# Optimization experiments

Hardware: AMD Instinct MI355X
Metric: run time of the kernel (lower is better)

Reference implementation:

```python
import jax, jax.numpy as jnp
import numpy as np

B, L, Q = 1024, 200, 1
DQ, DF = 512, 128
H, D1, D2 = 4, 128, 64


def setup_inputs() -> dict:
    key = jax.random.key(0)
    ks = jax.random.split(key, 20)
    inp = {
        "query": jax.random.normal(ks[0], (B, Q, DQ), jnp.float32),
        "fact": jax.random.normal(ks[1], (B, L, DF), jnp.float32),
        "mask": jax.random.randint(ks[2], (B, L), 0, 2, jnp.int32),
        "mm_cosine": jax.random.normal(ks[3], (2, B, L), jnp.float32),
    }
    # per-head FCRepeat weights, init per reset_parameters: randn/sqrt(fan_in), bias 0.1
    def w(k, fan_in, fan_out):
        return jax.random.normal(k, (H, fan_in, fan_out), jnp.float32) / np.sqrt(fan_in).astype(np.float32)
    inp["Wq1"] = w(ks[4], DQ, D1); inp["bq1"] = jnp.full((H, D1), 0.1, jnp.float32)
    inp["Wq2"] = w(ks[5], D1, D2); inp["bq2"] = jnp.full((H, D2), 0.1, jnp.float32)
    inp["Wf1"] = w(ks[6], DF, D1); inp["bf1"] = jnp.full((H, D1), 0.1, jnp.float32)
    inp["Wf2"] = w(ks[7], D1, D2); inp["bf2"] = jnp.full((H, D2), 0.1, jnp.float32)
    inp["Wv1"] = w(ks[8], DF, D1); inp["bv1"] = jnp.full((H, D1), 0.1, jnp.float32)
    inp["Wv2"] = w(ks[9], D1, D2); inp["bv2"] = jnp.full((H, D2), 0.1, jnp.float32)
    inp["tau1"] = jnp.full((2, H), 0.1, jnp.float32)   # cosine_tau1
    inp["tau2"] = jnp.full((3, H), 1.0, jnp.float32)   # cosine_tau2
    return inp


def _silu(x):
    return x * jax.nn.sigmoid(x)


def reference(query, fact, mask, mm_cosine,
              Wq1, bq1, Wq2, bq2, Wf1, bf1, Wf2, bf2, Wv1, bv1, Wv2, bv2,
              tau1, tau2):
    # per-head FC stacks (identity acts inside FCRepeat), then SiLU gating
    fq = jnp.einsum('bqi,hio->hbqo', query, Wq1) + bq1[:, None, None, :]
    fq = jnp.einsum('hbqi,hio->hbqo', fq, Wq2) + bq2[:, None, None, :]
    fq = _silu(fq)                                   # [H,B,1,D2]
    ff = jnp.einsum('bli,hio->hblo', fact, Wf1) + bf1[:, None, None, :]
    ff = jnp.einsum('hbli,hio->hblo', ff, Wf2) + bf2[:, None, None, :]
    ff = _silu(ff)                                   # [H,B,L,D2]
    fv = jnp.einsum('bli,hio->hblo', fact, Wv1) + bv1[:, None, None, :]
    fv = jnp.einsum('hbli,hio->hblo', fv, Wv2) + bv2[:, None, None, :]
    fv = _silu(fv)                                   # [H,B,L,D2]

    dot = jnp.einsum('hbld,hbqd->hblq', ff, fq)      # [H,B,L,1]
    dot = dot + (-1e9) * (1.0 - mask.astype(jnp.float32))[None, :, :, None]

    # cosine-bias cross terms
    bias = (mm_cosine[0][None] / tau1[0][:, None, None]
            + mm_cosine[1][None] / tau1[1][:, None, None])[..., None]  # [H,B,L,1]
    b1, b2, b3 = (tau2[i][:, None, None, None] for i in range(3))
    dot = b1 * dot + b2 * bias + b3 * dot * bias

    alphas = jax.nn.softmax(dot, axis=2) + 1e-7      # softmax over L
    out = jnp.einsum('hbld,hblq->hbdq', fv, alphas)[..., 0]  # [H,B,D2]
    return jnp.transpose(out, (1, 0, 2)).reshape(out.shape[1], -1)  # [B,H*D2]
```

## Files before the change

kernel.cpp:

```cpp
#include <hip/hip_runtime.h>
#include <hip/hip_bf16.h>

typedef __attribute__((ext_vector_type(8))) short short8;
typedef __attribute__((ext_vector_type(4))) float f32x4;

#define NH   4
#define NB   1024
#define NL   200
#define NDQ  512
#define NDF  128
#define ND1  128
#define ND2  64
#define LPAD 208
#define KP   136

#define OFF_WQC   0
#define OFF_BQC   (NH*NDQ*ND2*4)
#define OFF_FQ    (OFF_BQC + NH*ND2*4)
#define OFF_WIMG  (OFF_FQ + NH*NB*ND2*4)
#define OFF_BFC   (OFF_WIMG + NH*3*ND2*KP*2)
#define OFF_BVC   (OFF_BFC + NH*ND2*4)

__device__ inline short f2bf(float f) {
    union { float f; unsigned u; } v; v.f = f;
    unsigned r = (v.u + 0x7FFFu + ((v.u >> 16) & 1u)) >> 16;
    return (short)r;
}
__device__ inline float bf2f(short s) {
    union { unsigned u; float f; } v; v.u = ((unsigned)(unsigned short)s) << 16;
    return v.f;
}
__device__ inline float fsilu(float z) {
    return z * __fdividef(1.f, 1.f + __expf(-z));
}

__global__ __launch_bounds__(256) void k_combine(
    const float* __restrict__ Wq1, const float* __restrict__ bq1,
    const float* __restrict__ Wq2, const float* __restrict__ bq2,
    const float* __restrict__ Wf1, const float* __restrict__ bf1,
    const float* __restrict__ Wf2, const float* __restrict__ bf2,
    const float* __restrict__ Wv1, const float* __restrict__ bv1,
    const float* __restrict__ Wv2, const float* __restrict__ bv2,
    float* __restrict__ WQC, float* __restrict__ BQC,
    __hip_bfloat16* __restrict__ WIMG, float* __restrict__ BFC, float* __restrict__ BVC)
{
    int g = blockIdx.x * 256 + threadIdx.x;
    if (g < NH*NDQ*ND2) {
        int h = g >> 15, r = g & 32767, i = r >> 6, j = r & 63;
        const float* a  = Wq1 + (h*NDQ + i)*ND1;
        const float* bb = Wq2 + h*ND1*ND2 + j;
        float s = 0.f;
        for (int k = 0; k < ND1; ++k) s += a[k] * bb[k*ND2];
        WQC[(h*NDQ + i)*ND2 + j] = s;
        return;
    }
    g -= NH*NDQ*ND2;
    if (g < 2*NH*NDF*ND2) {
        int which = (g >= NH*NDF*ND2);
        int r0 = g & (NH*NDF*ND2 - 1);
        int h = r0 >> 13, r = r0 & 8191, i = r >> 6, j = r & 63;
        const float* W1 = (which ? Wv1 : Wf1) + (h*NDF + i)*ND1;
        const float* W2 = (which ? Wv2 : Wf2) + h*ND1*ND2 + j;
        float s = 0.f;
        for (int k = 0; k < ND1; ++k) s += W1[k] * W2[k*ND2];
        short hi = f2bf(s);
        short lo = f2bf(s - bf2f(hi));
        __hip_bfloat16* img = WIMG + (size_t)((h*3 + (which ? 2 : 0))*ND2 + j)*KP + i;
        ((short*)img)[0] = hi;
        if (!which) ((short*)img)[ND2*KP] = lo;
        return;
    }
    g -= 2*NH*NDF*ND2;
    if (g < NH*ND2) {
        int h = g >> 6, j = g & 63;
        float s = bq2[h*ND2 + j];
        for (int k = 0; k < ND1; ++k) s += bq1[h*ND1 + k] * Wq2[(h*ND1 + k)*ND2 + j];
        BQC[g] = s; return;
    }
    g -= NH*ND2;
    if (g < NH*ND2) {
        int h = g >> 6, j = g & 63;
        float s = bf2[h*ND2 + j];
        for (int k = 0; k < ND1; ++k) s += bf1[h*ND1 + k] * Wf2[(h*ND1 + k)*ND2 + j];
        BFC[g] = s; return;
    }
    g -= NH*ND2;
    if (g < NH*ND2) {
        int h = g >> 6, j = g & 63;
        float s = bv2[h*ND2 + j];
        for (int k = 0; k < ND1; ++k) s += bv1[h*ND1 + k] * Wv2[(h*ND1 + k)*ND2 + j];
        BVC[g] = s; return;
    }
}

__global__ __launch_bounds__(256) void k_fq(
    const float* __restrict__ query, const float* __restrict__ WQC,
    const float* __restrict__ BQC, float* __restrict__ FQ)
{
    __shared__ __align__(16) float qS[4*NDQ];
    const int t = threadIdx.x;
    const int b0 = blockIdx.x * 4;
    {
        const float4* src = (const float4*)(query + (size_t)b0 * NDQ);
        float4* dst = (float4*)qS;
        dst[t] = src[t];
        dst[t + 256] = src[t + 256];
    }
    __syncthreads();
    const int h = t >> 6, d = t & 63;
    float s0, s1, s2, s3;
    s0 = s1 = s2 = s3 = BQC[h*ND2 + d];
    const float* wp = WQC + (size_t)h*NDQ*ND2 + d;
    #pragma unroll 8
    for (int i = 0; i < NDQ; ++i) {
        float wv = wp[i*ND2];
        s0 += qS[i]        * wv;
        s1 += qS[NDQ + i]  * wv;
        s2 += qS[2*NDQ + i]* wv;
        s3 += qS[3*NDQ + i]* wv;
    }
    float* o = FQ + ((size_t)h*NB + b0)*ND2 + d;
    o[0]      = fsilu(s0);
    o[ND2]    = fsilu(s1);
    o[2*ND2]  = fsilu(s2);
    o[3*ND2]  = fsilu(s3);
}

__global__ __launch_bounds__(512, 2) void k_main(
    const float* __restrict__ fact,
    const int* __restrict__ mask,
    const float* __restrict__ mmc,
    const float* __restrict__ tau1,
    const float* __restrict__ tau2,
    const float* __restrict__ FQ,
    const float* __restrict__ BFC,
    const float* __restrict__ BVC,
    const __hip_bfloat16* __restrict__ WIMG,
    float* __restrict__ out)
{
    __shared__ __align__(16) __hip_bfloat16 wS[3*ND2*KP];
    __shared__ __align__(16) float dotS[LPAD];
    __shared__ __align__(16) float outPartS[512];

    const int t    = threadIdx.x;
    const int b    = blockIdx.x;
    const int w    = t >> 6;
    const int lane = t & 63;
    const int a15  = lane & 15;
    const int quad = lane >> 4;
    const int nmt  = (w < 5) ? 2 : 1;

    short8 afh[2][4], afl[2][4];
    const short8 zero8 = {0,0,0,0,0,0,0,0};
    for (int mi = 0; mi < 2; ++mi) {
        int mt = w + 8*mi;
        int row = mt*16 + a15;
        for (int kk = 0; kk < 4; ++kk) {
            short8 vh = zero8, vl = zero8;
            if (mt < 13 && row < NL) {
                const float* p = fact + ((size_t)(b*NL + row))*NDF + kk*32 + quad*8;
                float4 x0 = *(const float4*)p;
                float4 x1 = *(const float4*)(p + 4);
                float v[8] = {x0.x, x0.y, x0.z, x0.w, x1.x, x1.y, x1.z, x1.w};
                for (int j = 0; j < 8; ++j) {
                    short hs = f2bf(v[j]);
                    vh[j] = hs;
                    vl[j] = f2bf(v[j] - bf2f(hs));
                }
            }
            afh[mi][kk] = vh;
            afl[mi][kk] = vl;
        }
    }

    const int bL = b * NL;
    const f32x4 zf = {0.f, 0.f, 0.f, 0.f};

    for (int h = 0; h < NH; ++h) {
        __syncthreads();
        if (h > 0 && t < 64) {
            float s = 0.f;
            for (int ww = 0; ww < 8; ++ww) s += outPartS[ww*64 + t];
            out[(size_t)b*(NH*ND2) + (h-1)*ND2 + t] = s;
        }
        {
            const float4* src = (const float4*)(WIMG + (size_t)(h*3)*ND2*KP);
            float4* dst = (float4*)wS;
            for (int i = t; i < 3264; i += 512) dst[i] = src[i];
        }
        float fqv[4], bfcv[4], bvcv[4];
        for (int nt = 0; nt < 4; ++nt) {
            int col = nt*16 + a15;
            fqv[nt]  = FQ[((size_t)h*NB + b)*ND2 + col];
            bfcv[nt] = BFC[h*ND2 + col];
            bvcv[nt] = BVC[h*ND2 + col];
        }
        const float t1a = tau1[h];
        const float t1b = tau1[NH + h];
        const float t20 = tau2[h];
        const float t21 = tau2[NH + h];
        const float t22 = tau2[2*NH + h];
        __syncthreads();

        f32x4 acc[2][4];
        for (int mi = 0; mi < 2; ++mi) for (int nt = 0; nt < 4; ++nt) acc[mi][nt] = zf;
        for (int kk = 0; kk < 4; ++kk) {
            short8 bh[4], bl[4];
            for (int nt = 0; nt < 4; ++nt) {
                const __hip_bfloat16* p = wS + (nt*16 + a15)*KP + kk*32 + quad*8;
                bh[nt] = *(const short8*)p;
                bl[nt] = *(const short8*)(p + ND2*KP);
            }
            for (int mi = 0; mi < 2; ++mi)
                if (mi < nmt)
                    for (int nt = 0; nt < 4; ++nt) {
                        acc[mi][nt] = __builtin_amdgcn_mfma_f32_16x16x32_bf16(afh[mi][kk], bh[nt], acc[mi][nt], 0, 0, 0);
                        acc[mi][nt] = __builtin_amdgcn_mfma_f32_16x16x32_bf16(afh[mi][kk], bl[nt], acc[mi][nt], 0, 0, 0);
                        acc[mi][nt] = __builtin_amdgcn_mfma_f32_16x16x32_bf16(afl[mi][kk], bh[nt], acc[mi][nt], 0, 0, 0);
                    }
        }

        for (int mi = 0; mi < 2; ++mi)
            if (mi < nmt) {
                int mt = w + 8*mi;
                for (int rg = 0; rg < 4; ++rg) {
                    float s = 0.f;
                    for (int nt = 0; nt < 4; ++nt)
                        s += fsilu(acc[mi][nt][rg] + bfcv[nt]) * fqv[nt];
                    s += __shfl_xor(s, 1);
                    s += __shfl_xor(s, 2);
                    s += __shfl_xor(s, 4);
                    s += __shfl_xor(s, 8);
                    if (a15 == rg) dotS[mt*16 + quad*4 + rg] = s;
                }
            }
        __syncthreads();

        float lg[4];
        float vmax = -3.0e38f;
        #pragma unroll
        for (int j = 0; j < 4; ++j) {
            int r = lane + 64*j;
            float l = -3.0e38f;
            if (r < NL) {
                float dv = dotS[r] - 1e9f * (1.0f - (float)mask[bL + r]);
                float bias = __fdividef(mmc[bL + r], t1a) + __fdividef(mmc[NB*NL + bL + r], t1b);
                l = t20*dv + t21*bias + t22*dv*bias;
            }
            lg[j] = l;
            vmax = fmaxf(vmax, l);
        }
        #pragma unroll
        for (int off = 1; off < 64; off <<= 1) vmax = fmaxf(vmax, __shfl_xor(vmax, off));
        float vsum = 0.f;
        #pragma unroll
        for (int j = 0; j < 4; ++j)
            if (lane + 64*j < NL) vsum += __expf(lg[j] - vmax);
        #pragma unroll
        for (int off = 1; off < 64; off <<= 1) vsum += __shfl_xor(vsum, off);
        const float rdenom = __fdividef(1.f, vsum);

        float al[2][4];
        for (int mi = 0; mi < 2; ++mi)
            for (int rg = 0; rg < 4; ++rg) {
                float a = 0.f;
                if (mi < nmt) {
                    int r = (w + 8*mi)*16 + quad*4 + rg;
                    if (r < NL) {
                        float dv = dotS[r] - 1e9f * (1.0f - (float)mask[bL + r]);
                        float bias = __fdividef(mmc[bL + r], t1a) + __fdividef(mmc[NB*NL + bL + r], t1b);
                        float l = t20*dv + t21*bias + t22*dv*bias;
                        a = __expf(l - vmax) * rdenom + 1e-7f;
                    }
                }
                al[mi][rg] = a;
            }

        for (int mi = 0; mi < 2; ++mi) for (int nt = 0; nt < 4; ++nt) acc[mi][nt] = zf;
        for (int kk = 0; kk < 4; ++kk) {
            short8 bh[4];
            for (int nt = 0; nt < 4; ++nt)
                bh[nt] = *(const short8*)(wS + (2*ND2 + nt*16 + a15)*KP + kk*32 + quad*8);
            for (int mi = 0; mi < 2; ++mi)
                if (mi < nmt)
                    for (int nt = 0; nt < 4; ++nt)
                        acc[mi][nt] = __builtin_amdgcn_mfma_f32_16x16x32_bf16(afh[mi][kk], bh[nt], acc[mi][nt], 0, 0, 0);
        }

        float o[4] = {0.f, 0.f, 0.f, 0.f};
        for (int mi = 0; mi < 2; ++mi)
            if (mi < nmt)
                for (int rg = 0; rg < 4; ++rg)
                    for (int nt = 0; nt < 4; ++nt)
                        o[nt] += al[mi][rg] * fsilu(acc[mi][nt][rg] + bvcv[nt]);
        for (int nt = 0; nt < 4; ++nt) {
            o[nt] += __shfl_xor(o[nt], 16);
            o[nt] += __shfl_xor(o[nt], 32);
        }
        if (lane < 16)
            for (int nt = 0; nt < 4; ++nt) outPartS[w*64 + nt*16 + lane] = o[nt];
    }
    __syncthreads();
    if (t < 64) {
        float s = 0.f;
        for (int ww = 0; ww < 8; ++ww) s += outPartS[ww*64 + t];
        out[(size_t)b*(NH*ND2) + (NH-1)*ND2 + t] = s;
    }
}

extern "C" void kernel_launch(void* const* d_in, const int* in_sizes, int n_in,
                              void* d_out, int out_size, void* d_ws, size_t ws_size,
                              hipStream_t stream) {
    const float* query = (const float*)d_in[0];
    const float* fact  = (const float*)d_in[1];
    const int*   maskp = (const int*)d_in[2];
    const float* mmc   = (const float*)d_in[3];
    const float* Wq1 = (const float*)d_in[4];
    const float* bq1 = (const float*)d_in[5];
    const float* Wq2 = (const float*)d_in[6];
    const float* bq2 = (const float*)d_in[7];
    const float* Wf1 = (const float*)d_in[8];
    const float* bf1 = (const float*)d_in[9];
    const float* Wf2 = (const float*)d_in[10];
    const float* bf2 = (const float*)d_in[11];
    const float* Wv1 = (const float*)d_in[12];
    const float* bv1 = (const float*)d_in[13];
    const float* Wv2 = (const float*)d_in[14];
    const float* bv2 = (const float*)d_in[15];
    const float* tau1 = (const float*)d_in[16];
    const float* tau2 = (const float*)d_in[17];

    char* ws = (char*)d_ws;
    float*          WQC  = (float*)(ws + OFF_WQC);
    float*          BQC  = (float*)(ws + OFF_BQC);
    float*          FQ   = (float*)(ws + OFF_FQ);
    __hip_bfloat16* WIMG = (__hip_bfloat16*)(ws + OFF_WIMG);
    float*          BFC  = (float*)(ws + OFF_BFC);
    float*          BVC  = (float*)(ws + OFF_BVC);

    k_combine<<<771, 256, 0, stream>>>(Wq1, bq1, Wq2, bq2, Wf1, bf1, Wf2, bf2,
                                       Wv1, bv1, Wv2, bv2, WQC, BQC, WIMG, BFC, BVC);
    k_fq<<<NB/4, 256, 0, stream>>>(query, WQC, BQC, FQ);
    k_main<<<NB, 512, 0, stream>>>(fact, maskp, mmc, tau1, tau2, FQ, BFC, BVC, WIMG,
                                   (float*)d_out);
}
```

Measured before the change: 385.5 us.

## Use per-wave partial softmax merge and cut block barriers in attention kernel

The main kernel no longer writes logits to shared memory and runs a block-wide softmax. Each wave now computes a local max and sum-of-exps and an unnormalized weighted value sum, and one small cross-wave merge per head combines them. This removes several barriers per head. The next head's weights are loaded into LDS after the merge, the launch-bound occupancy hint goes up, MFMA loops get raised scheduling priority, and k_fq uses smaller blocks with more of them. In exchange the kernel adds extra register pressure under the higher occupancy target and must carry the +1e-7 term as a separate masked sum.

```diff
diff --git a/kernel.cpp b/kernel.cpp
--- a/kernel.cpp
+++ b/kernel.cpp
@@ -11,7 +11,6 @@
 #define NDF  128
 #define ND1  128
 #define ND2  64
-#define LPAD 208
 #define KP   136
 
 #define OFF_WQC   0
@@ -97,36 +96,30 @@
     const float* __restrict__ query, const float* __restrict__ WQC,
     const float* __restrict__ BQC, float* __restrict__ FQ)
 {
-    __shared__ __align__(16) float qS[4*NDQ];
+    __shared__ __align__(16) float qS[2*NDQ];
     const int t = threadIdx.x;
-    const int b0 = blockIdx.x * 4;
+    const int b0 = blockIdx.x * 2;
     {
         const float4* src = (const float4*)(query + (size_t)b0 * NDQ);
-        float4* dst = (float4*)qS;
-        dst[t] = src[t];
-        dst[t + 256] = src[t + 256];
+        ((float4*)qS)[t] = src[t];
     }
     __syncthreads();
     const int h = t >> 6, d = t & 63;
-    float s0, s1, s2, s3;
-    s0 = s1 = s2 = s3 = BQC[h*ND2 + d];
+    float s0, s1;
+    s0 = s1 = BQC[h*ND2 + d];
     const float* wp = WQC + (size_t)h*NDQ*ND2 + d;
-    #pragma unroll 8
+    #pragma unroll 16
     for (int i = 0; i < NDQ; ++i) {
         float wv = wp[i*ND2];
-        s0 += qS[i]        * wv;
-        s1 += qS[NDQ + i]  * wv;
-        s2 += qS[2*NDQ + i]* wv;
-        s3 += qS[3*NDQ + i]* wv;
+        s0 += qS[i]       * wv;
+        s1 += qS[NDQ + i] * wv;
     }
     float* o = FQ + ((size_t)h*NB + b0)*ND2 + d;
-    o[0]      = fsilu(s0);
-    o[ND2]    = fsilu(s1);
-    o[2*ND2]  = fsilu(s2);
-    o[3*ND2]  = fsilu(s3);
-}
-
-__global__ __launch_bounds__(512, 2) void k_main(
+    o[0]   = fsilu(s0);
+    o[ND2] = fsilu(s1);
+}
+
+__global__ __launch_bounds__(512, 4) void k_main(
     const float* __restrict__ fact,
     const int* __restrict__ mask,
     const float* __restrict__ mmc,
@@ -139,8 +132,7 @@
     float* __restrict__ out)
 {
     __shared__ __align__(16) __hip_bfloat16 wS[3*ND2*KP];
-    __shared__ __align__(16) float dotS[LPAD];
-    __shared__ __align__(16) float outPartS[512];
+    __shared__ __align__(16) float pS[8][132];
 
     const int t    = threadIdx.x;
     const int b    = blockIdx.x;
@@ -176,34 +168,23 @@
     const int bL = b * NL;
     const f32x4 zf = {0.f, 0.f, 0.f, 0.f};
 
+    {
+        const float4* src = (const float4*)(WIMG);
+        float4* dst = (float4*)wS;
+        for (int i = t; i < 3264; i += 512) dst[i] = src[i];
+    }
+    __syncthreads();
+
     for (int h = 0; h < NH; ++h) {
-        __syncthreads();
-        if (h > 0 && t < 64) {
-            float s = 0.f;
-            for (int ww = 0; ww < 8; ++ww) s += outPartS[ww*64 + t];
-            out[(size_t)b*(NH*ND2) + (h-1)*ND2 + t] = s;
-        }
-        {
-            const float4* src = (const float4*)(WIMG + (size_t)(h*3)*ND2*KP);
-            float4* dst = (float4*)wS;
-            for (int i = t; i < 3264; i += 512) dst[i] = src[i];
-        }
-        float fqv[4], bfcv[4], bvcv[4];
-        for (int nt = 0; nt < 4; ++nt) {
-            int col = nt*16 + a15;
-            fqv[nt]  = FQ[((size_t)h*NB + b)*ND2 + col];
-            bfcv[nt] = BFC[h*ND2 + col];
-            bvcv[nt] = BVC[h*ND2 + col];
-        }
-        const float t1a = tau1[h];
-        const float t1b = tau1[NH + h];
+        const float rt1a = __fdividef(1.f, tau1[h]);
+        const float rt1b = __fdividef(1.f, tau1[NH + h]);
         const float t20 = tau2[h];
         const float t21 = tau2[NH + h];
         const float t22 = tau2[2*NH + h];
-        __syncthreads();
 
         f32x4 acc[2][4];
         for (int mi = 0; mi < 2; ++mi) for (int nt = 0; nt < 4; ++nt) acc[mi][nt] = zf;
+        __builtin_amdgcn_s_setprio(1);
         for (int kk = 0; kk < 4; ++kk) {
             short8 bh[4], bl[4];
             for (int nt = 0; nt < 4; ++nt) {
@@ -219,11 +200,19 @@
                         acc[mi][nt] = __builtin_amdgcn_mfma_f32_16x16x32_bf16(afl[mi][kk], bh[nt], acc[mi][nt], 0, 0, 0);
                     }
         }
-
+        __builtin_amdgcn_s_setprio(0);
+
+        float fqv[4], bfcv[4];
+        for (int nt = 0; nt < 4; ++nt) {
+            int col = nt*16 + a15;
+            fqv[nt]  = FQ[((size_t)h*NB + b)*ND2 + col];
+            bfcv[nt] = BFC[h*ND2 + col];
+        }
+        float lg[2][4];
         for (int mi = 0; mi < 2; ++mi)
-            if (mi < nmt) {
-                int mt = w + 8*mi;
-                for (int rg = 0; rg < 4; ++rg) {
+            for (int rg = 0; rg < 4; ++rg) {
+                float l = -3.0e38f;
+                if (mi < nmt) {
                     float s = 0.f;
                     for (int nt = 0; nt < 4; ++nt)
                         s += fsilu(acc[mi][nt][rg] + bfcv[nt]) * fqv[nt];
@@ -231,52 +220,34 @@
                     s += __shfl_xor(s, 2);
                     s += __shfl_xor(s, 4);
                     s += __shfl_xor(s, 8);
-                    if (a15 == rg) dotS[mt*16 + quad*4 + rg] = s;
+                    int r = (w + 8*mi)*16 + quad*4 + rg;
+                    if (r < NL) {
+                        float dv = s - 1e9f * (1.0f - (float)mask[bL + r]);
+                        float bias = mmc[bL + r]*rt1a + mmc[NB*NL + bL + r]*rt1b;
+                        l = t20*dv + t21*bias + t22*dv*bias;
+                    }
                 }
-            }
-        __syncthreads();
-
-        float lg[4];
-        float vmax = -3.0e38f;
-        #pragma unroll
-        for (int j = 0; j < 4; ++j) {
-            int r = lane + 64*j;
-            float l = -3.0e38f;
-            if (r < NL) {
-                float dv = dotS[r] - 1e9f * (1.0f - (float)mask[bL + r]);
-                float bias = __fdividef(mmc[bL + r], t1a) + __fdividef(mmc[NB*NL + bL + r], t1b);
-                l = t20*dv + t21*bias + t22*dv*bias;
-            }
-            lg[j] = l;
-            vmax = fmaxf(vmax, l);
-        }
-        #pragma unroll
-        for (int off = 1; off < 64; off <<= 1) vmax = fmaxf(vmax, __shfl_xor(vmax, off));
-        float vsum = 0.f;
-        #pragma unroll
-        for (int j = 0; j < 4; ++j)
-            if (lane + 64*j < NL) vsum += __expf(lg[j] - vmax);
-        #pragma unroll
-        for (int off = 1; off < 64; off <<= 1) vsum += __shfl_xor(vsum, off);
-        const float rdenom = __fdividef(1.f, vsum);
-
-        float al[2][4];
+                lg[mi][rg] = l;
+            }
+
+        float m = lg[0][0];
+        m = fmaxf(m, lg[0][1]); m = fmaxf(m, lg[0][2]); m = fmaxf(m, lg[0][3]);
+        m = fmaxf(m, lg[1][0]); m = fmaxf(m, lg[1][1]);
+        m = fmaxf(m, lg[1][2]); m = fmaxf(m, lg[1][3]);
+        m = fmaxf(m, __shfl_xor(m, 16));
+        m = fmaxf(m, __shfl_xor(m, 32));
+        float sw = 0.f;
         for (int mi = 0; mi < 2; ++mi)
             for (int rg = 0; rg < 4; ++rg) {
-                float a = 0.f;
-                if (mi < nmt) {
-                    int r = (w + 8*mi)*16 + quad*4 + rg;
-                    if (r < NL) {
-                        float dv = dotS[r] - 1e9f * (1.0f - (float)mask[bL + r]);
-                        float bias = __fdividef(mmc[bL + r], t1a) + __fdividef(mmc[NB*NL + bL + r], t1b);
-                        float l = t20*dv + t21*bias + t22*dv*bias;
-                        a = __expf(l - vmax) * rdenom + 1e-7f;
-                    }
-                }
-                al[mi][rg] = a;
-            }
+                float p = __expf(lg[mi][rg] - m);
+                lg[mi][rg] = p;
+                sw += p;
+            }
+        sw += __shfl_xor(sw, 16);
+        sw += __shfl_xor(sw, 32);
 
         for (int mi = 0; mi < 2; ++mi) for (int nt = 0; nt < 4; ++nt) acc[mi][nt] = zf;
+        __builtin_amdgcn_s_setprio(1);
         for (int kk = 0; kk < 4; ++kk) {
             short8 bh[4];
             for (int nt = 0; nt < 4; ++nt)
@@ -286,25 +257,55 @@
                     for (int nt = 0; nt < 4; ++nt)
                         acc[mi][nt] = __builtin_amdgcn_mfma_f32_16x16x32_bf16(afh[mi][kk], bh[nt], acc[mi][nt], 0, 0, 0);
         }
-
-        float o[4] = {0.f, 0.f, 0.f, 0.f};
+        __builtin_amdgcn_s_setprio(0);
+
+        float bvcv[4];
+        for (int nt = 0; nt < 4; ++nt) bvcv[nt] = BVC[h*ND2 + nt*16 + a15];
+        float oE[4] = {0.f,0.f,0.f,0.f}, oS[4] = {0.f,0.f,0.f,0.f};
         for (int mi = 0; mi < 2; ++mi)
             if (mi < nmt)
-                for (int rg = 0; rg < 4; ++rg)
-                    for (int nt = 0; nt < 4; ++nt)
-                        o[nt] += al[mi][rg] * fsilu(acc[mi][nt][rg] + bvcv[nt]);
+                for (int rg = 0; rg < 4; ++rg) {
+                    float p = lg[mi][rg];
+                    int r = (w + 8*mi)*16 + quad*4 + rg;
+                    float vm = (r < NL) ? 1.f : 0.f;
+                    for (int nt = 0; nt < 4; ++nt) {
+                        float sv = fsilu(acc[mi][nt][rg] + bvcv[nt]);
+                        oE[nt] += p * sv;
+                        oS[nt] += vm * sv;
+                    }
+                }
         for (int nt = 0; nt < 4; ++nt) {
-            o[nt] += __shfl_xor(o[nt], 16);
-            o[nt] += __shfl_xor(o[nt], 32);
-        }
-        if (lane < 16)
-            for (int nt = 0; nt < 4; ++nt) outPartS[w*64 + nt*16 + lane] = o[nt];
-    }
-    __syncthreads();
-    if (t < 64) {
-        float s = 0.f;
-        for (int ww = 0; ww < 8; ++ww) s += outPartS[ww*64 + t];
-        out[(size_t)b*(NH*ND2) + (NH-1)*ND2 + t] = s;
+            oE[nt] += __shfl_xor(oE[nt], 16);
+            oE[nt] += __shfl_xor(oE[nt], 32);
+            oS[nt] += __shfl_xor(oS[nt], 16);
+            oS[nt] += __shfl_xor(oS[nt], 32);
+        }
+        if (lane == 0) { pS[w][0] = m; pS[w][1] = sw; }
+        if (quad == 0)
+            for (int nt = 0; nt < 4; ++nt) {
+                pS[w][2  + nt*16 + a15] = oE[nt];
+                pS[w][66 + nt*16 + a15] = oS[nt];
+            }
+        __syncthreads();
+
+        if (h + 1 < NH) {
+            const float4* src = (const float4*)(WIMG + (size_t)((h+1)*3)*ND2*KP);
+            float4* dst = (float4*)wS;
+            for (int i = t; i < 3264; i += 512) dst[i] = src[i];
+        }
+        if (t < 64) {
+            float M = pS[0][0];
+            for (int ww = 1; ww < 8; ++ww) M = fmaxf(M, pS[ww][0]);
+            float den = 0.f, num = 0.f, s1 = 0.f;
+            for (int ww = 0; ww < 8; ++ww) {
+                float e = __expf(pS[ww][0] - M);
+                den += e * pS[ww][1];
+                num += e * pS[ww][2 + t];
+                s1  += pS[ww][66 + t];
+            }
+            out[(size_t)b*(NH*ND2) + h*ND2 + t] = num * __fdividef(1.f, den) + 1e-7f * s1;
+        }
+        __syncthreads();
     }
 }
 
@@ -340,7 +341,7 @@
 
     k_combine<<<771, 256, 0, stream>>>(Wq1, bq1, Wq2, bq2, Wf1, bf1, Wf2, bf2,
                                        Wv1, bv1, Wv2, bv2, WQC, BQC, WIMG, BFC, BVC);
-    k_fq<<<NB/4, 256, 0, stream>>>(query, WQC, BQC, FQ);
+    k_fq<<<NB/2, 256, 0, stream>>>(query, WQC, BQC, FQ);
     k_main<<<NB, 512, 0, stream>>>(fact, maskp, mmc, tau1, tau2, FQ, BFC, BVC, WIMG,
                                    (float*)d_out);
 }
```

Measured after the change: 407.1 us. 5.6% more time.
